# Kernel tuning notes

Hardware: AMD Instinct MI355X
Metric: run time of the kernel (lower is better)

## Reference

```python
import jax, jax.numpy as jnp
import numpy as np

N_BITS = 16
V = 1 << N_BITS  # 65536 possible 16-bit patterns


def setup_inputs() -> dict:
    key = jax.random.key(0)
    k1, k2, k3 = jax.random.split(key, 3)
    B, H, T = 16, 128, 4096
    W = jax.random.normal(k1, (B, H, N_BITS), dtype=jnp.float32) * 0.5  # per-bit weights
    r = jax.random.normal(k2, (B, H), dtype=jnp.float32)                 # per-hidden phase/bias
    # x holds raw 16-bit patterns (indices into the 2^16 support)
    x = jax.random.randint(k3, (B, T), 0, V, dtype=jnp.int32)
    return {"x": x, "W": W, "r": r}


def _logits_all(W, r):
    """Logit of every one of the 2^16 representable values. [B, V]"""
    enum = jnp.arange(V, dtype=jnp.int32)
    shifts = jnp.arange(N_BITS, dtype=jnp.int32)
    bits = ((enum[:, None] >> shifts[None, :]) & 1).astype(W.dtype)  # [V, N]
    z = jnp.einsum('vn,bhn->bvh', bits, W) + r[:, None, :]           # [B, V, H]
    return jnp.cos(z).sum(axis=-1)                                    # [B, V]


def reference(x, W, r):
    """BIDE forward: log_prob(x) = logit(bits(x)) - logsumexp over all 2^N patterns."""
    logits = _logits_all(W, r)                       # [B, V]
    logZ = jax.nn.logsumexp(logits, axis=1)          # [B]  exact partition over full support
    logit_x = jnp.take_along_axis(logits, x, axis=1) # [B, T] gather by bit-pattern index
    return logit_x - logZ[:, None]
```

## Files before the change

kernel.cpp:

```cpp
#include <hip/hip_runtime.h>
#include <hip/hip_bf16.h>

#define BDIM 16
#define HDIM 128
#define TDIM 4096
#define VSZ  65536
#define NTAB (BDIM * HDIM * 256)

__global__ __launch_bounds__(256) void bide_tables(
    const float* __restrict__ W, const float* __restrict__ r,
    float* __restrict__ tabAre, float* __restrict__ tabAim,
    float* __restrict__ tabBre, float* __restrict__ tabBim) {
  int bh = blockIdx.x;
  const float* Wp = W + bh * 16;
  float rv = r[bh];
  int t = threadIdx.x;

  float slo = rv;
  float shi = 0.f;
#pragma unroll
  for (int n = 0; n < 8; ++n) {
    float bit = (float)((t >> n) & 1);
    slo = fmaf(bit, Wp[n], slo);
    shi = fmaf(bit, Wp[8 + n], shi);
  }
  float sl, cl, sh, ch;
  __sincosf(slo, &sl, &cl);
  __sincosf(shi, &sh, &ch);
  int o = bh * 256 + t;
  tabAre[o] = cl;  tabAim[o] = sl;
  tabBre[o] = ch;  tabBim[o] = sh;
}

__global__ __launch_bounds__(256) void bide_logits(
    const float* __restrict__ tabAre, const float* __restrict__ tabAim,
    const float* __restrict__ tabBre, const float* __restrict__ tabBim,
    float* __restrict__ logits) {
  __shared__ float lAre[32][64];
  __shared__ float lAim[32][64];
  __shared__ float lBre[32][64];
  __shared__ float lBim[32][64];

  int bid = blockIdx.x;
  int b    = bid >> 4;
  int tile = bid & 15;
  int tlo = (tile & 3) * 64;
  int thi = (tile >> 2) * 64;
  int tid = threadIdx.x;
  int tx = tid & 15;
  int ty = tid >> 4;

  const float* Ar = tabAre + b * HDIM * 256;
  const float* Ai = tabAim + b * HDIM * 256;
  const float* Br = tabBre + b * HDIM * 256;
  const float* Bi = tabBim + b * HDIM * 256;

  float acc[4][4] = {};

  for (int kc = 0; kc < 4; ++kc) {
#pragma unroll
    for (int i = 0; i < 8; ++i) {
      int idx = tid + i * 256;
      int row = idx >> 6, col = idx & 63;
      int g = (kc * 32 + row) * 256;
      lAre[row][col] = Ar[g + tlo + col];
      lAim[row][col] = Ai[g + tlo + col];
      lBre[row][col] = Br[g + thi + col];
      lBim[row][col] = Bi[g + thi + col];
    }
    __syncthreads();

#pragma unroll 4
    for (int h = 0; h < 32; ++h) {
      float4 ar4 = *(const float4*)(&lAre[h][tx * 4]);
      float4 ai4 = *(const float4*)(&lAim[h][tx * 4]);
      float4 br4 = *(const float4*)(&lBre[h][ty * 4]);
      float4 bi4 = *(const float4*)(&lBim[h][ty * 4]);
      float arr[4] = {ar4.x, ar4.y, ar4.z, ar4.w};
      float aii[4] = {ai4.x, ai4.y, ai4.z, ai4.w};
      float brr[4] = {br4.x, br4.y, br4.z, br4.w};
      float bii[4] = {bi4.x, bi4.y, bi4.z, bi4.w};
#pragma unroll
      for (int i = 0; i < 4; ++i)
#pragma unroll
        for (int j = 0; j < 4; ++j) {
          acc[i][j] = fmaf(brr[i], arr[j], acc[i][j]);
          acc[i][j] = fmaf(-bii[i], aii[j], acc[i][j]);
        }
    }
    __syncthreads();
  }

  float* Lb = logits + b * VSZ;
#pragma unroll
  for (int i = 0; i < 4; ++i) {
    int hi = thi + ty * 4 + i;
    float4 v = make_float4(acc[i][0], acc[i][1], acc[i][2], acc[i][3]);
    *(float4*)(&Lb[hi * 256 + tlo + tx * 4]) = v;
  }
}

__global__ __launch_bounds__(256) void bide_lse_part(
    const float* __restrict__ logits,
    float* __restrict__ partM, float* __restrict__ partS) {
  int bid = blockIdx.x;
  int b = bid >> 5, c = bid & 31;
  const float* L = logits + b * VSZ + c * 2048;
  int tid = threadIdx.x;
  int lane = tid & 63, wid = tid >> 6;

  float v[8];
  float m = -1e30f;
#pragma unroll
  for (int i = 0; i < 8; ++i) {
    v[i] = L[tid + i * 256];
    m = fmaxf(m, v[i]);
  }
  __shared__ float wred[4];
  __shared__ float wsum[4];
#pragma unroll
  for (int off = 1; off < 64; off <<= 1) m = fmaxf(m, __shfl_xor(m, off, 64));
  if (lane == 0) wred[wid] = m;
  __syncthreads();
  float M = fmaxf(fmaxf(wred[0], wred[1]), fmaxf(wred[2], wred[3]));

  float s = 0.f;
#pragma unroll
  for (int i = 0; i < 8; ++i) s += __expf(v[i] - M);
#pragma unroll
  for (int off = 1; off < 64; off <<= 1) s += __shfl_xor(s, off, 64);
  if (lane == 0) wsum[wid] = s;
  __syncthreads();
  if (tid == 0) {
    partM[b * 32 + c] = M;
    partS[b * 32 + c] = wsum[0] + wsum[1] + wsum[2] + wsum[3];
  }
}

__global__ __launch_bounds__(256) void bide_out(
    const float* __restrict__ logits,
    const float* __restrict__ partM, const float* __restrict__ partS,
    const int* __restrict__ x, float* __restrict__ out) {
  int bid = blockIdx.x;
  int b = bid >> 4;
  int t0 = (bid & 15) * 256;
  int tid = threadIdx.x;

  __shared__ float s_logZ;
  if (tid < 64) {
    float m = (tid < 32) ? partM[b * 32 + tid] : -1e30f;
    float M = m;
#pragma unroll
    for (int off = 1; off < 64; off <<= 1) M = fmaxf(M, __shfl_xor(M, off, 64));
    float s = (tid < 32) ? partS[b * 32 + tid] * __expf(m - M) : 0.f;
#pragma unroll
    for (int off = 1; off < 64; off <<= 1) s += __shfl_xor(s, off, 64);
    if (tid == 0) s_logZ = M + __logf(s);
  }
  __syncthreads();
  float logZ = s_logZ;

  int t = t0 + tid;
  int vidx = x[b * TDIM + t];
  out[b * TDIM + t] = logits[b * VSZ + vidx] - logZ;
}

extern "C" void kernel_launch(void* const* d_in, const int* in_sizes, int n_in,
                              void* d_out, int out_size, void* d_ws, size_t ws_size,
                              hipStream_t stream) {
  const int*   x = (const int*)d_in[0];
  const float* W = (const float*)d_in[1];
  const float* r = (const float*)d_in[2];
  float* out = (float*)d_out;

  float* tabAre = (float*)d_ws;
  float* tabAim = tabAre + NTAB;
  float* tabBre = tabAim + NTAB;
  float* tabBim = tabBre + NTAB;
  float* logits = tabBim + NTAB;
  float* partM  = logits + BDIM * VSZ;
  float* partS  = partM + BDIM * 32;

  bide_tables<<<BDIM * HDIM, 256, 0, stream>>>(W, r, tabAre, tabAim, tabBre, tabBim);
  bide_logits<<<BDIM * 16, 256, 0, stream>>>(tabAre, tabAim, tabBre, tabBim, logits);
  bide_lse_part<<<BDIM * 32, 256, 0, stream>>>(logits, partM, partS);
  bide_out<<<BDIM * TDIM / 256, 256, 0, stream>>>(logits, partM, partS, x, out);
}
```

Before: 84.49 us.

## Fuse sincos tables into logits kernel and merge logsumexp with gather

Each logits block now computes the cos/sin factor tables it needs directly into shared memory, which removes the table kernel and its global round-trip. Blocks go from 256 to 512 threads with a 2x4 per-thread output tile. The partial-logsumexp and gather kernels are merged into one kernel with one 1024-thread block per batch that reads the logits twice. This cuts two launches and the intermediate buffers, at the cost of only 16 blocks for the reduction stage and redundant sincos work across tiles.

```diff
diff --git a/kernel.cpp b/kernel.cpp
--- a/kernel.cpp
+++ b/kernel.cpp
@@ -5,36 +5,9 @@
 #define HDIM 128
 #define TDIM 4096
 #define VSZ  65536
-#define NTAB (BDIM * HDIM * 256)
 
-__global__ __launch_bounds__(256) void bide_tables(
+__global__ __launch_bounds__(512) void bide_fused_logits(
     const float* __restrict__ W, const float* __restrict__ r,
-    float* __restrict__ tabAre, float* __restrict__ tabAim,
-    float* __restrict__ tabBre, float* __restrict__ tabBim) {
-  int bh = blockIdx.x;
-  const float* Wp = W + bh * 16;
-  float rv = r[bh];
-  int t = threadIdx.x;
-
-  float slo = rv;
-  float shi = 0.f;
-#pragma unroll
-  for (int n = 0; n < 8; ++n) {
-    float bit = (float)((t >> n) & 1);
-    slo = fmaf(bit, Wp[n], slo);
-    shi = fmaf(bit, Wp[8 + n], shi);
-  }
-  float sl, cl, sh, ch;
-  __sincosf(slo, &sl, &cl);
-  __sincosf(shi, &sh, &ch);
-  int o = bh * 256 + t;
-  tabAre[o] = cl;  tabAim[o] = sl;
-  tabBre[o] = ch;  tabBim[o] = sh;
-}
-
-__global__ __launch_bounds__(256) void bide_logits(
-    const float* __restrict__ tabAre, const float* __restrict__ tabAim,
-    const float* __restrict__ tabBre, const float* __restrict__ tabBim,
     float* __restrict__ logits) {
   __shared__ float lAre[32][64];
   __shared__ float lAim[32][64];
@@ -47,45 +20,60 @@
   int tlo = (tile & 3) * 64;
   int thi = (tile >> 2) * 64;
   int tid = threadIdx.x;
+  int lane6 = tid & 63;
+  int wrow  = tid >> 6;
   int tx = tid & 15;
   int ty = tid >> 4;
 
-  const float* Ar = tabAre + b * HDIM * 256;
-  const float* Ai = tabAim + b * HDIM * 256;
-  const float* Br = tabBre + b * HDIM * 256;
-  const float* Bi = tabBim + b * HDIM * 256;
+  const float* Wb = W + b * HDIM * 16;
+  const float* rb = r + b * HDIM;
 
-  float acc[4][4] = {};
+  float acc[2][4] = {};
 
   for (int kc = 0; kc < 4; ++kc) {
+    int hbase = kc * 32;
 #pragma unroll
-    for (int i = 0; i < 8; ++i) {
-      int idx = tid + i * 256;
-      int row = idx >> 6, col = idx & 63;
-      int g = (kc * 32 + row) * 256;
-      lAre[row][col] = Ar[g + tlo + col];
-      lAim[row][col] = Ai[g + tlo + col];
-      lBre[row][col] = Br[g + thi + col];
-      lBim[row][col] = Bi[g + thi + col];
+    for (int i = 0; i < 4; ++i) {
+      int row = wrow + i * 8;
+      int h = hbase + row;
+      const float* Wp = Wb + h * 16;
+      int va = tlo + lane6;
+      float sa = rb[h];
+#pragma unroll
+      for (int n = 0; n < 8; ++n)
+        sa = fmaf((float)((va >> n) & 1), Wp[n], sa);
+      float sina, cosa;
+      __sincosf(sa, &sina, &cosa);
+      lAre[row][lane6] = cosa;
+      lAim[row][lane6] = sina;
+      int vb = thi + lane6;
+      float sb = 0.f;
+#pragma unroll
+      for (int n = 0; n < 8; ++n)
+        sb = fmaf((float)((vb >> n) & 1), Wp[8 + n], sb);
+      float sinb, cosb;
+      __sincosf(sb, &sinb, &cosb);
+      lBre[row][lane6] = cosb;
+      lBim[row][lane6] = sinb;
     }
     __syncthreads();
 
 #pragma unroll 4
     for (int h = 0; h < 32; ++h) {
-      float4 ar4 = *(const float4*)(&lAre[h][tx * 4]);
-      float4 ai4 = *(const float4*)(&lAim[h][tx * 4]);
-      float4 br4 = *(const float4*)(&lBre[h][ty * 4]);
-      float4 bi4 = *(const float4*)(&lBim[h][ty * 4]);
-      float arr[4] = {ar4.x, ar4.y, ar4.z, ar4.w};
-      float aii[4] = {ai4.x, ai4.y, ai4.z, ai4.w};
-      float brr[4] = {br4.x, br4.y, br4.z, br4.w};
-      float bii[4] = {bi4.x, bi4.y, bi4.z, bi4.w};
+      float4 ar = *(const float4*)&lAre[h][tx * 4];
+      float4 ai = *(const float4*)&lAim[h][tx * 4];
+      float2 br = *(const float2*)&lBre[h][ty * 2];
+      float2 bi = *(const float2*)&lBim[h][ty * 2];
+      float arr[4] = {ar.x, ar.y, ar.z, ar.w};
+      float aii[4] = {ai.x, ai.y, ai.z, ai.w};
+      float brr[2] = {br.x, br.y};
+      float bii[2] = {bi.x, bi.y};
 #pragma unroll
-      for (int i = 0; i < 4; ++i)
+      for (int i2 = 0; i2 < 2; ++i2)
 #pragma unroll
         for (int j = 0; j < 4; ++j) {
-          acc[i][j] = fmaf(brr[i], arr[j], acc[i][j]);
-          acc[i][j] = fmaf(-bii[i], aii[j], acc[i][j]);
+          acc[i2][j] = fmaf(brr[i2], arr[j], acc[i2][j]);
+          acc[i2][j] = fmaf(-bii[i2], aii[j], acc[i2][j]);
         }
     }
     __syncthreads();
@@ -93,76 +81,65 @@
 
   float* Lb = logits + b * VSZ;
 #pragma unroll
-  for (int i = 0; i < 4; ++i) {
-    int hi = thi + ty * 4 + i;
-    float4 v = make_float4(acc[i][0], acc[i][1], acc[i][2], acc[i][3]);
-    *(float4*)(&Lb[hi * 256 + tlo + tx * 4]) = v;
+  for (int i2 = 0; i2 < 2; ++i2) {
+    int hi = thi + ty * 2 + i2;
+    float4 v = make_float4(acc[i2][0], acc[i2][1], acc[i2][2], acc[i2][3]);
+    *(float4*)&Lb[hi * 256 + tlo + tx * 4] = v;
   }
 }
 
-__global__ __launch_bounds__(256) void bide_lse_part(
-    const float* __restrict__ logits,
-    float* __restrict__ partM, float* __restrict__ partS) {
-  int bid = blockIdx.x;
-  int b = bid >> 5, c = bid & 31;
-  const float* L = logits + b * VSZ + c * 2048;
+__global__ __launch_bounds__(1024) void bide_lse_gather(
+    const float* __restrict__ logits, const int* __restrict__ x,
+    float* __restrict__ out) {
+  int b = blockIdx.x;
   int tid = threadIdx.x;
   int lane = tid & 63, wid = tid >> 6;
+  const float4* L4 = (const float4*)(logits + b * VSZ);
+  __shared__ float wred[16];
+  __shared__ float s_logZ;
 
-  float v[8];
   float m = -1e30f;
 #pragma unroll
-  for (int i = 0; i < 8; ++i) {
-    v[i] = L[tid + i * 256];
-    m = fmaxf(m, v[i]);
+  for (int i = 0; i < 16; ++i) {
+    float4 v = L4[tid + i * 1024];
+    m = fmaxf(fmaxf(fmaxf(m, v.x), v.y), fmaxf(v.z, v.w));
   }
-  __shared__ float wred[4];
-  __shared__ float wsum[4];
 #pragma unroll
   for (int off = 1; off < 64; off <<= 1) m = fmaxf(m, __shfl_xor(m, off, 64));
   if (lane == 0) wred[wid] = m;
   __syncthreads();
-  float M = fmaxf(fmaxf(wred[0], wred[1]), fmaxf(wred[2], wred[3]));
+  float M = wred[0];
+#pragma unroll
+  for (int i = 1; i < 16; ++i) M = fmaxf(M, wred[i]);
+  __syncthreads();
 
   float s = 0.f;
 #pragma unroll
-  for (int i = 0; i < 8; ++i) s += __expf(v[i] - M);
+  for (int i = 0; i < 16; ++i) {
+    float4 v = L4[tid + i * 1024];
+    s += __expf(v.x - M) + __expf(v.y - M) + __expf(v.z - M) + __expf(v.w - M);
+  }
 #pragma unroll
   for (int off = 1; off < 64; off <<= 1) s += __shfl_xor(s, off, 64);
-  if (lane == 0) wsum[wid] = s;
+  if (lane == 0) wred[wid] = s;
   __syncthreads();
   if (tid == 0) {
-    partM[b * 32 + c] = M;
-    partS[b * 32 + c] = wsum[0] + wsum[1] + wsum[2] + wsum[3];
-  }
-}
-
-__global__ __launch_bounds__(256) void bide_out(
-    const float* __restrict__ logits,
-    const float* __restrict__ partM, const float* __restrict__ partS,
-    const int* __restrict__ x, float* __restrict__ out) {
-  int bid = blockIdx.x;
-  int b = bid >> 4;
-  int t0 = (bid & 15) * 256;
-  int tid = threadIdx.x;
-
-  __shared__ float s_logZ;
-  if (tid < 64) {
-    float m = (tid < 32) ? partM[b * 32 + tid] : -1e30f;
-    float M = m;
+    float S = 0.f;
 #pragma unroll
-    for (int off = 1; off < 64; off <<= 1) M = fmaxf(M, __shfl_xor(M, off, 64));
-    float s = (tid < 32) ? partS[b * 32 + tid] * __expf(m - M) : 0.f;
-#pragma unroll
-    for (int off = 1; off < 64; off <<= 1) s += __shfl_xor(s, off, 64);
-    if (tid == 0) s_logZ = M + __logf(s);
+    for (int i = 0; i < 16; ++i) S += wred[i];
+    s_logZ = M + __logf(S);
   }
   __syncthreads();
   float logZ = s_logZ;
 
-  int t = t0 + tid;
-  int vidx = x[b * TDIM + t];
-  out[b * TDIM + t] = logits[b * VSZ + vidx] - logZ;
+  const float* Lb = logits + b * VSZ;
+  const int* xb = x + b * TDIM;
+  float* ob = out + b * TDIM;
+#pragma unroll
+  for (int i = 0; i < 4; ++i) {
+    int t = tid + i * 1024;
+    ob[t] = Lb[xb[t]] - logZ;
+  }
 }
 
 extern "C" void kernel_launch(void* const* d_in, const int* in_sizes, int n_in,
@@ -173,16 +150,8 @@
   const float* r = (const float*)d_in[2];
   float* out = (float*)d_out;
 
-  float* tabAre = (float*)d_ws;
-  float* tabAim = tabAre + NTAB;
-  float* tabBre = tabAim + NTAB;
-  float* tabBim = tabBre + NTAB;
-  float* logits = tabBim + NTAB;
-  float* partM  = logits + BDIM * VSZ;
-  float* partS  = partM + BDIM * 32;
+  float* logits = (float*)d_ws;
 
-  bide_tables<<<BDIM * HDIM, 256, 0, stream>>>(W, r, tabAre, tabAim, tabBre, tabBim);
-  bide_logits<<<BDIM * 16, 256, 0, stream>>>(tabAre, tabAim, tabBre, tabBim, logits);
-  bide_lse_part<<<BDIM * 32, 256, 0, stream>>>(logits, partM, partS);
-  bide_out<<<BDIM * TDIM / 256, 256, 0, stream>>>(logits, partM, partS, x, out);
+  bide_fused_logits<<<BDIM * 16, 512, 0, stream>>>(W, r, logits);
+  bide_lse_gather<<<BDIM, 1024, 0, stream>>>(logits, x, out);
 }
```

Result: no change. 83.37 us (-1.3%).
